# Kernel optimization log

Measured on AMD Instinct MI355X. Metric: run time of the kernel, lower is better.

The kernel has to match this reference:

```python
import jax, jax.numpy as jnp
import numpy as np

D_MODEL = 1024
NUM_HEADS = 16
NUM_KV_HEADS = 4
HEAD_DIM = D_MODEL // NUM_HEADS  # 64
THETA = 10000.0
MAX_SEQ_LEN = 4096


def _rope_tables(max_seq_len, d_k, theta):
    k_vec = jnp.arange(0, d_k, 2, dtype=jnp.float32) / d_k
    freq = 1.0 / (theta ** k_vec)                       # (d_k/2,)
    ang = jnp.arange(max_seq_len, dtype=jnp.float32)[:, None] * freq[None, :]
    return jnp.cos(ang), jnp.sin(ang)                   # each (max_seq_len, d_k/2)


def _apply_rope(x, pos, cos_table, sin_table):
    # x: (b, h, l, d), pos: (b, l)
    cos = cos_table[pos][:, None, :, :]                 # (b, 1, l, d/2)
    sin = sin_table[pos][:, None, :, :]
    even, odd = x[..., 0::2], x[..., 1::2]
    r1 = even * cos - odd * sin
    r2 = even * sin + odd * cos
    return jnp.stack([r1, r2], axis=-1).reshape(x.shape)  # interleave back


def setup_inputs() -> dict:
    key = jax.random.key(0)
    ks = jax.random.split(key, 6)
    B, L, D = 1, 4096, D_MODEL
    std = (2.0 / (D + D)) ** 0.5
    std_kv = (2.0 / (D + HEAD_DIM * NUM_KV_HEADS)) ** 0.5
    x = jax.random.normal(ks[0], (B, L, D), dtype=jnp.float32)
    Wq = jax.random.normal(ks[1], (D, D), dtype=jnp.float32) * std
    Wk = jax.random.normal(ks[2], (HEAD_DIM * NUM_KV_HEADS, D), dtype=jnp.float32) * std_kv
    Wv = jax.random.normal(ks[3], (HEAD_DIM * NUM_KV_HEADS, D), dtype=jnp.float32) * std_kv
    Wo = jax.random.normal(ks[4], (D, D), dtype=jnp.float32) * std
    token_positions = jnp.broadcast_to(jnp.arange(L, dtype=jnp.int32), (B, L))
    return {"x": x, "Wq": Wq, "Wk": Wk, "Wv": Wv, "Wo": Wo,
            "token_positions": token_positions}


def reference(x, Wq, Wk, Wv, Wo, token_positions):
    B, L, D = x.shape
    H, Hkv, Dh = NUM_HEADS, NUM_KV_HEADS, HEAD_DIM
    n_rep = H // Hkv
    cos_t, sin_t = _rope_tables(MAX_SEQ_LEN, Dh, THETA)

    q = (x @ Wq.T).reshape(B, L, H, Dh).transpose(0, 2, 1, 3)      # b h l d
    k = (x @ Wk.T).reshape(B, L, Hkv, Dh).transpose(0, 2, 1, 3)    # b g l d
    v = (x @ Wv.T).reshape(B, L, Hkv, Dh).transpose(0, 2, 1, 3)

    q = _apply_rope(q, token_positions, cos_t, sin_t)
    k = _apply_rope(k, token_positions, cos_t, sin_t)

    # GQA: group query heads by kv head
    qg = q.reshape(B, Hkv, n_rep, L, Dh)
    scores = jnp.einsum('bgrqd,bgkd->bgrqk', qg, k) / jnp.sqrt(jnp.float32(Dh))
    causal = jnp.tril(jnp.ones((L, L), dtype=bool))
    scores = jnp.where(causal, scores, -jnp.inf)
    weights = jax.nn.softmax(scores, axis=-1)
    out = jnp.einsum('bgrqk,bgkd->bgrqd', weights, v)              # b g r q d
    out = out.reshape(B, H, L, Dh).transpose(0, 2, 1, 3).reshape(B, L, D)
    return out @ Wo.T
```

## Files before the change

### kernel.cpp

```cpp
#include <hip/hip_runtime.h>
#include <hip/hip_bf16.h>
#include <math.h>

typedef __bf16 bf16;
typedef __bf16 v8bf __attribute__((ext_vector_type(8)));
typedef __bf16 v4bf __attribute__((ext_vector_type(4)));
typedef __bf16 v2bf __attribute__((ext_vector_type(2)));
typedef float f32x4 __attribute__((ext_vector_type(4)));
typedef float f32x16 __attribute__((ext_vector_type(16)));

#define L_SEQ 4096
#define DMODEL 1024
#define NHEADS 16
#define DH 64
#define NEG_BIG (-1e30f)
#define LN1E4_64 0.14391156f
#define SCL2 0.18033688f
#define DEFER_THR 8.0f

static __device__ __forceinline__ unsigned pkbf(float x, float y) {
    v2bf t; t[0] = (bf16)x; t[1] = (bf16)y;
    return __builtin_bit_cast(unsigned, t);
}

__global__ void convert_all(const float* __restrict__ x, const float* __restrict__ wq,
                            const float* __restrict__ wk, const float* __restrict__ wv,
                            const float* __restrict__ wo,
                            bf16* __restrict__ xb, bf16* __restrict__ wqkvb,
                            bf16* __restrict__ wob) {
    int i = (blockIdx.x * 256 + threadIdx.x) * 4;
    const float* src;
    bf16* dst;
    if (i < 4194304)      { src = x  + i;             dst = xb    + i; }
    else if (i < 5242880) { src = wq + (i - 4194304); dst = wqkvb + (i - 4194304); }
    else if (i < 5505024) { src = wk + (i - 5242880); dst = wqkvb + 1048576 + (i - 5242880); }
    else if (i < 5767168) { src = wv + (i - 5505024); dst = wqkvb + 1310720 + (i - 5505024); }
    else                  { src = wo + (i - 5767168); dst = wob   + (i - 5767168); }
    f32x4 v = *(const f32x4*)src;
    v4bf r;
#pragma unroll
    for (int j = 0; j < 4; j++) r[j] = (bf16)v[j];
    *(v4bf*)dst = r;
}

__global__ __launch_bounds__(512) void gemm_qkv(const bf16* __restrict__ A,
                                                const bf16* __restrict__ W,
                                                bf16* __restrict__ Qb,
                                                bf16* __restrict__ Kb,
                                                bf16* __restrict__ Vtg,
                                                const int* __restrict__ tp) {
    __shared__ bf16 As[128][68];
    __shared__ bf16 Bs[128][68];
    const int K = 1024;
    const int tid = threadIdx.x;
    const int w = tid >> 6, lane = tid & 63;
    const int quad = lane >> 4, l16 = lane & 15;
    const int wm = (w & 1) * 64, wn = (w >> 1) * 32;
    const int bm = blockIdx.y * 128, bn = blockIdx.x * 128;

    f32x4 acc[4][2];
#pragma unroll
    for (int mf = 0; mf < 4; mf++)
#pragma unroll
        for (int nf = 0; nf < 2; nf++) acc[mf][nf] = (f32x4){0.f, 0.f, 0.f, 0.f};

    const int sr = tid >> 2;
    const int scb = (tid & 3) * 16;

    v8bf pa0, pa1, pb0, pb1;
    {
        const bf16* ap = &A[(size_t)(bm + sr) * K + scb];
        const bf16* bp = &W[(size_t)(bn + sr) * K + scb];
        pa0 = *(const v8bf*)ap; pa1 = *(const v8bf*)(ap + 8);
        pb0 = *(const v8bf*)bp; pb1 = *(const v8bf*)(bp + 8);
        *(v8bf*)&As[sr][scb] = pa0; *(v8bf*)&As[sr][scb + 8] = pa1;
        *(v8bf*)&Bs[sr][scb] = pb0; *(v8bf*)&Bs[sr][scb + 8] = pb1;
    }

    for (int kt = 0; kt < K; kt += 64) {
        __syncthreads();
        const bool more = (kt + 64) < K;
        if (more) {
            const bf16* ap = &A[(size_t)(bm + sr) * K + kt + 64 + scb];
            const bf16* bp = &W[(size_t)(bn + sr) * K + kt + 64 + scb];
            pa0 = *(const v8bf*)ap; pa1 = *(const v8bf*)(ap + 8);
            pb0 = *(const v8bf*)bp; pb1 = *(const v8bf*)(bp + 8);
        }
#pragma unroll
        for (int kf = 0; kf < 2; kf++) {
            v8bf a[4], b[2];
#pragma unroll
            for (int mf = 0; mf < 4; mf++) a[mf] = *(v8bf*)&As[wm + mf * 16 + l16][kf * 32 + quad * 8];
#pragma unroll
            for (int nf = 0; nf < 2; nf++) b[nf] = *(v8bf*)&Bs[wn + nf * 16 + l16][kf * 32 + quad * 8];
#pragma unroll
            for (int mf = 0; mf < 4; mf++)
#pragma unroll
                for (int nf = 0; nf < 2; nf++)
                    acc[mf][nf] = __builtin_amdgcn_mfma_f32_16x16x32_bf16(a[mf], b[nf], acc[mf][nf], 0, 0, 0);
        }
        __syncthreads();
        if (more) {
            *(v8bf*)&As[sr][scb] = pa0; *(v8bf*)&As[sr][scb + 8] = pa1;
            *(v8bf*)&Bs[sr][scb] = pb0; *(v8bf*)&Bs[sr][scb + 8] = pb1;
        }
    }

    if (bn < 1024) {
#pragma unroll
        for (int mf = 0; mf < 4; mf++) {
            int pos_[4];
#pragma unroll
            for (int r = 0; r < 4; r++) pos_[r] = tp[bm + wm + mf * 16 + quad * 4 + r];
#pragma unroll
            for (int nf = 0; nf < 2; nf++) {
                const int col = bn + wn + nf * 16 + l16;
                float fr = __expf(-(float)((col & 63) & ~1) * LN1E4_64);
#pragma unroll
                for (int r = 0; r < 4; r++) {
                    float v = acc[mf][nf][r];
                    float sn, cs;
                    __sincosf((float)pos_[r] * fr, &sn, &cs);
                    float p = __shfl_xor(v, 1);
                    float res = (l16 & 1) ? (p * sn + v * cs) : (v * cs - p * sn);
                    int row = bm + wm + mf * 16 + quad * 4 + r;
                    Qb[(size_t)row * DMODEL + col] = (bf16)(res * SCL2);
                }
            }
        }
    } else if (bn < 1280) {
#pragma unroll
        for (int mf = 0; mf < 4; mf++) {
            int pos_[4];
#pragma unroll
            for (int r = 0; r < 4; r++) pos_[r] = tp[bm + wm + mf * 16 + quad * 4 + r];
#pragma unroll
            for (int nf = 0; nf < 2; nf++) {
                const int kcol = bn - 1024 + wn + nf * 16 + l16;
                float fr = __expf(-(float)((kcol & 63) & ~1) * LN1E4_64);
#pragma unroll
                for (int r = 0; r < 4; r++) {
                    float v = acc[mf][nf][r];
                    float sn, cs;
                    __sincosf((float)pos_[r] * fr, &sn, &cs);
                    float p = __shfl_xor(v, 1);
                    float res = (l16 & 1) ? (p * sn + v * cs) : (v * cs - p * sn);
                    int row = bm + wm + mf * 16 + quad * 4 + r;
                    Kb[(size_t)row * 256 + kcol] = (bf16)res;
                }
            }
        }
    } else {
#pragma unroll
        for (int mf = 0; mf < 4; mf++)
#pragma unroll
            for (int nf = 0; nf < 2; nf++) {
                v4bf pk;
#pragma unroll
                for (int r = 0; r < 4; r++) pk[r] = (bf16)acc[mf][nf][r];
                int vcol = bn - 1280 + wn + nf * 16 + l16;
                int row = bm + wm + mf * 16 + quad * 4;
                *(v4bf*)&Vtg[(size_t)vcol * L_SEQ + row] = pk;
            }
    }
}

__global__ __launch_bounds__(512) void gemm_out(const bf16* __restrict__ A,
                                                const bf16* __restrict__ W,
                                                float* __restrict__ C) {
    __shared__ bf16 As[128][68];
    __shared__ bf16 Bs[128][68];
    const int K = 1024, N = 1024;
    const int tid = threadIdx.x;
    const int w = tid >> 6, lane = tid & 63;
    const int quad = lane >> 4, l16 = lane & 15;
    const int wm = (w & 1) * 64, wn = (w >> 1) * 32;
    const int bm = blockIdx.y * 128, bn = blockIdx.x * 128;

    f32x4 acc[4][2];
#pragma unroll
    for (int mf = 0; mf < 4; mf++)
#pragma unroll
        for (int nf = 0; nf < 2; nf++) acc[mf][nf] = (f32x4){0.f, 0.f, 0.f, 0.f};

    const int sr = tid >> 2;
    const int scb = (tid & 3) * 16;

    v8bf pa0, pa1, pb0, pb1;
    {
        const bf16* ap = &A[(size_t)(bm + sr) * K + scb];
        const bf16* bp = &W[(size_t)(bn + sr) * K + scb];
        pa0 = *(const v8bf*)ap; pa1 = *(const v8bf*)(ap + 8);
        pb0 = *(const v8bf*)bp; pb1 = *(const v8bf*)(bp + 8);
        *(v8bf*)&As[sr][scb] = pa0; *(v8bf*)&As[sr][scb + 8] = pa1;
        *(v8bf*)&Bs[sr][scb] = pb0; *(v8bf*)&Bs[sr][scb + 8] = pb1;
    }

    for (int kt = 0; kt < K; kt += 64) {
        __syncthreads();
        const bool more = (kt + 64) < K;
        if (more) {
            const bf16* ap = &A[(size_t)(bm + sr) * K + kt + 64 + scb];
            const bf16* bp = &W[(size_t)(bn + sr) * K + kt + 64 + scb];
            pa0 = *(const v8bf*)ap; pa1 = *(const v8bf*)(ap + 8);
            pb0 = *(const v8bf*)bp; pb1 = *(const v8bf*)(bp + 8);
        }
#pragma unroll
        for (int kf = 0; kf < 2; kf++) {
            v8bf a[4], b[2];
#pragma unroll
            for (int mf = 0; mf < 4; mf++) a[mf] = *(v8bf*)&As[wm + mf * 16 + l16][kf * 32 + quad * 8];
#pragma unroll
            for (int nf = 0; nf < 2; nf++) b[nf] = *(v8bf*)&Bs[wn + nf * 16 + l16][kf * 32 + quad * 8];
#pragma unroll
            for (int mf = 0; mf < 4; mf++)
#pragma unroll
                for (int nf = 0; nf < 2; nf++)
                    acc[mf][nf] = __builtin_amdgcn_mfma_f32_16x16x32_bf16(a[mf], b[nf], acc[mf][nf], 0, 0, 0);
        }
        __syncthreads();
        if (more) {
            *(v8bf*)&As[sr][scb] = pa0; *(v8bf*)&As[sr][scb + 8] = pa1;
            *(v8bf*)&Bs[sr][scb] = pb0; *(v8bf*)&Bs[sr][scb + 8] = pb1;
        }
    }
#pragma unroll
    for (int mf = 0; mf < 4; mf++)
#pragma unroll
        for (int nf = 0; nf < 2; nf++)
#pragma unroll
            for (int r = 0; r < 4; r++) {
                int row = bm + wm + mf * 16 + quad * 4 + r;
                int col = bn + wn + nf * 16 + l16;
                C[(size_t)row * N + col] = acc[mf][nf][r];
            }
}

__global__ __launch_bounds__(256, 2) void flash10(const bf16* __restrict__ Q,
                                                  const bf16* __restrict__ Kb,
                                                  const bf16* __restrict__ Vtg,
                                                  bf16* __restrict__ O0,
                                                  bf16* __restrict__ O1,
                                                  float* __restrict__ ML) {
    __shared__ bf16 Ks[128][68];
    __shared__ bf16 Vt[64][132];
    const int h = blockIdx.y, kvh = h >> 2;
    const int bx = blockIdx.x;
    const int tid = threadIdx.x;
    const int w = tid >> 6, lane = tid & 63;
    const int l32 = lane & 31, hi = lane >> 5;
    const int krow = tid >> 1, kcb = (tid & 1) * 32;
    const int vr = tid >> 2, vcb = (tid & 3) * 32;

    for (int p = 0; p < 2; p++) {
        const int qb = p ? (31 - bx) : bx;
        const int T = qb + 1;
        const int k0 = p ? ((T + 1) >> 1) : 0;
        const int k1 = p ? T : ((T + 1) >> 1);
        bf16* Op = p ? O1 : O0;
        float* mlp = ML + (size_t)(p * NHEADS + h) * L_SEQ * 2;

        if (k0 >= k1) {
            for (int i = tid; i < 128 * 64; i += 256) {
                int rr = i >> 6, cc = i & 63;
                Op[(size_t)(qb * 128 + rr) * DMODEL + h * DH + cc] = (bf16)0.f;
            }
            if (tid < 128) {
                mlp[(qb * 128 + tid) * 2 + 0] = NEG_BIG;
                mlp[(qb * 128 + tid) * 2 + 1] = 0.f;
            }
            continue;
        }

        const int qrow = qb * 128 + w * 32 + l32;
        v8bf qf[4];
#pragma unroll
        for (int d16 = 0; d16 < 4; d16++)
            qf[d16] = *(const v8bf*)&Q[(size_t)qrow * DMODEL + h * DH + d16 * 16 + hi * 8];

        f32x16 oaccT[2];
#pragma unroll
        for (int d = 0; d < 2; d++)
#pragma unroll
            for (int r = 0; r < 16; r++) oaccT[d][r] = 0.f;
        float m_i = NEG_BIG, l_i = 0.f;

        v8bf kreg[4], vreg[4];
        {
            const bf16* ks = &Kb[(size_t)(k0 * 128 + krow) * 256 + kvh * DH + kcb];
            const bf16* vs = &Vtg[(size_t)(kvh * DH + vr) * L_SEQ + k0 * 128 + vcb];
#pragma unroll
            for (int u = 0; u < 4; u++) { kreg[u] = *(const v8bf*)&ks[8 * u]; vreg[u] = *(const v8bf*)&vs[8 * u]; }
            __syncthreads();
#pragma unroll
            for (int u = 0; u < 4; u++) { *(v8bf*)&Ks[krow][kcb + 8 * u] = kreg[u]; *(v8bf*)&Vt[vr][vcb + 8 * u] = vreg[u]; }
        }

        for (int kb = k0; kb < k1; kb++) {
            __syncthreads();
            if (kb + 1 < k1) {
                const bf16* ks = &Kb[(size_t)((kb + 1) * 128 + krow) * 256 + kvh * DH + kcb];
                const bf16* vs = &Vtg[(size_t)(kvh * DH + vr) * L_SEQ + (kb + 1) * 128 + vcb];
#pragma unroll
                for (int u = 0; u < 4; u++) { kreg[u] = *(const v8bf*)&ks[8 * u]; vreg[u] = *(const v8bf*)&vs[8 * u]; }
            }

            f32x16 s[4];
            __builtin_amdgcn_s_setprio(1);
#pragma unroll
            for (int n = 0; n < 4; n++) {
#pragma unroll
                for (int r = 0; r < 16; r++) s[n][r] = 0.f;
#pragma unroll
                for (int d16 = 0; d16 < 4; d16++) {
                    v8bf av = *(v8bf*)&Ks[n * 32 + l32][d16 * 16 + hi * 8];
                    s[n] = __builtin_amdgcn_mfma_f32_32x32x16_bf16(av, qf[d16], s[n], 0, 0, 0);
                }
            }
            __builtin_amdgcn_s_setprio(0);

            if (kb == qb) {
#pragma unroll
                for (int n = 0; n < 4; n++) {
                    int kbase = kb * 128 + n * 32 + 4 * hi;
#pragma unroll
                    for (int r = 0; r < 16; r++) {
                        int key = kbase + (r & 3) + 8 * (r >> 2);
                        if (key > qrow) s[n][r] = NEG_BIG;
                    }
                }
            }

            float mx = NEG_BIG;
#pragma unroll
            for (int n = 0; n < 4; n++)
#pragma unroll
                for (int r = 0; r < 16; r += 2)
                    mx = fmaxf(fmaxf(mx, s[n][r]), s[n][r + 1]);
            mx = fmaxf(mx, __shfl_xor(mx, 32));

            if (!__all(mx <= m_i + DEFER_THR)) {
                float mnew = fmaxf(m_i, mx);
                float alpha = exp2f(m_i - mnew);
                l_i *= alpha;
#pragma unroll
                for (int d = 0; d < 2; d++)
#pragma unroll
                    for (int r = 0; r < 16; r++) oaccT[d][r] *= alpha;
                m_i = mnew;
            }

            float rs = 0.f;
#pragma unroll
            for (int n = 0; n < 4; n++)
#pragma unroll
                for (int r = 0; r < 16; r++) {
                    float pv = exp2f(s[n][r] - m_i);
                    s[n][r] = pv;
                    rs += pv;
                }
            rs += __shfl_xor(rs, 32);
            l_i += rs;

            __builtin_amdgcn_s_setprio(1);
#pragma unroll
            for (int n = 0; n < 4; n++) {
#pragma unroll
                for (int u = 0; u < 2; u++) {
                    const int ro = u * 8;
                    unsigned a0 = pkbf(s[n][ro + 0], s[n][ro + 1]);
                    unsigned a1 = pkbf(s[n][ro + 2], s[n][ro + 3]);
                    unsigned b0 = pkbf(s[n][ro + 4], s[n][ro + 5]);
                    unsigned b1 = pkbf(s[n][ro + 6], s[n][ro + 7]);
#if __has_builtin(__builtin_amdgcn_permlane32_swap)
                    auto s0 = __builtin_amdgcn_permlane32_swap(a0, b0, false, false);
                    auto s1 = __builtin_amdgcn_permlane32_swap(a1, b1, false, false);
                    unsigned w0 = s0[0], w2 = s0[1], w1 = s1[0], w3 = s1[1];
#else
                    unsigned t0 = hi ? a0 : b0;
                    unsigned r0 = __shfl_xor(t0, 32);
                    unsigned w0 = hi ? r0 : a0, w2 = hi ? b0 : r0;
                    unsigned t1 = hi ? a1 : b1;
                    unsigned r1 = __shfl_xor(t1, 32);
                    unsigned w1 = hi ? r1 : a1, w3 = hi ? b1 : r1;
#endif
                    union { unsigned uu[4]; v8bf v; } pf;
                    pf.uu[0] = w0; pf.uu[1] = w1; pf.uu[2] = w2; pf.uu[3] = w3;
                    const int t = n * 2 + u;
#pragma unroll
                    for (int dblk = 0; dblk < 2; dblk++) {
                        v8bf av = *(v8bf*)&Vt[dblk * 32 + l32][t * 16 + hi * 8];
                        oaccT[dblk] = __builtin_amdgcn_mfma_f32_32x32x16_bf16(av, pf.v, oaccT[dblk], 0, 0, 0);
                    }
                }
            }
            __builtin_amdgcn_s_setprio(0);

            __syncthreads();
            if (kb + 1 < k1) {
#pragma unroll
                for (int u = 0; u < 4; u++) { *(v8bf*)&Ks[krow][kcb + 8 * u] = kreg[u]; *(v8bf*)&Vt[vr][vcb + 8 * u] = vreg[u]; }
            }
        }

#pragma unroll
        for (int dblk = 0; dblk < 2; dblk++)
#pragma unroll
            for (int r = 0; r < 16; r++) {
                int d = dblk * 32 + (r & 3) + 8 * (r >> 2) + 4 * hi;
                Ks[w * 32 + l32][d] = (bf16)oaccT[dblk][r];
            }
        asm volatile("s_waitcnt lgkmcnt(0)" ::: "memory");
        __builtin_amdgcn_sched_barrier(0);
#pragma unroll
        for (int i = 0; i < 4; i++) {
            int cc = (lane & 1) * 32 + i * 8;
            int rr = w * 32 + (lane >> 1);
            v8bf ov = *(v8bf*)&Ks[rr][cc];
            *(v8bf*)&Op[(size_t)(qb * 128 + rr) * DMODEL + h * DH + cc] = ov;
        }
        if (hi == 0) {
            mlp[qrow * 2 + 0] = m_i;
            mlp[qrow * 2 + 1] = l_i;
        }
    }
}

__global__ void combine(const bf16* __restrict__ O0, const bf16* __restrict__ O1,
                        const float* __restrict__ ML, bf16* __restrict__ Attn) {
    int gid = blockIdx.x * 256 + threadIdx.x;
    int row = gid >> 8;
    int cg = (gid & 255) * 4;
    int h = cg >> 6;
    const float* ml0 = ML + ((size_t)h * L_SEQ + row) * 2;
    const float* ml1 = ML + ((size_t)(NHEADS + h) * L_SEQ + row) * 2;
    float m0 = ml0[0], l0 = ml0[1], m1 = ml1[0], l1 = ml1[1];
    float m = fmaxf(m0, m1);
    float a0 = exp2f(m0 - m), a1 = exp2f(m1 - m);
    float inv = 1.f / (a0 * l0 + a1 * l1);
    v4bf o0 = *(const v4bf*)&O0[(size_t)row * DMODEL + cg];
    v4bf o1 = *(const v4bf*)&O1[(size_t)row * DMODEL + cg];
    v4bf res;
#pragma unroll
    for (int j = 0; j < 4; j++)
        res[j] = (bf16)((a0 * (float)o0[j] + a1 * (float)o1[j]) * inv);
    *(v4bf*)&Attn[(size_t)row * DMODEL + cg] = res;
}

extern "C" void kernel_launch(void* const* d_in, const int* in_sizes, int n_in,
                              void* d_out, int out_size, void* d_ws, size_t ws_size,
                              hipStream_t stream) {
    const float* x  = (const float*)d_in[0];
    const float* Wq = (const float*)d_in[1];
    const float* Wk = (const float*)d_in[2];
    const float* Wv = (const float*)d_in[3];
    const float* Wo = (const float*)d_in[4];
    const int*   tp = (const int*)d_in[5];
    float* out = (float*)d_out;

    bf16*  xb    = (bf16*)d_ws;
    bf16*  wqkvb = xb    + 4194304;
    bf16*  wob   = wqkvb + 1572864;
    bf16*  Qb    = wob   + 1048576;
    bf16*  Kb    = Qb    + 4194304;
    bf16*  Vtg   = Kb    + 1048576;
    float* MLf   = (float*)(Vtg + 1048576);
    bf16*  Attn  = xb;
    bf16*  O0    = (bf16*)d_out;
    bf16*  O1    = O0 + 4194304;

    convert_all<<<6656, 256, 0, stream>>>(x, Wq, Wk, Wv, Wo, xb, wqkvb, wob);
    gemm_qkv<<<dim3(12, 32), 512, 0, stream>>>(xb, wqkvb, Qb, Kb, Vtg, tp);
    flash10<<<dim3(32, NHEADS), 256, 0, stream>>>(Qb, Kb, Vtg, O0, O1, MLf);
    combine<<<4096, 256, 0, stream>>>(O0, O1, MLf, Attn);
    gemm_out<<<dim3(8, 32), 512, 0, stream>>>(Attn, wob, out);
}
```

Before: 200.1 us.

## Double-buffer GEMM LDS tiles, swap grid order, compute softmax row-sum via MFMA

Both GEMMs now use double-buffered shared-memory tiles, so the next tile is written into the alternate buffer and each k-step needs one barrier instead of two. The launch grids of the GEMMs and the attention kernel are transposed, so consecutive blocks walk along M or across heads, which changes L2 reuse of the weight and KV tiles. The attention kernel drops the scalar row-sum and cross-lane shuffle and instead accumulates the softmax denominator with an extra MFMA against a vector of ones. This adds MFMA work, accumulator registers and doubled LDS usage, which may reduce occupancy.

```diff
diff --git a/kernel.cpp b/kernel.cpp
--- a/kernel.cpp
+++ b/kernel.cpp
@@ -49,14 +49,14 @@
                                                 bf16* __restrict__ Kb,
                                                 bf16* __restrict__ Vtg,
                                                 const int* __restrict__ tp) {
-    __shared__ bf16 As[128][68];
-    __shared__ bf16 Bs[128][68];
+    __shared__ bf16 As[2][128][68];
+    __shared__ bf16 Bs[2][128][68];
     const int K = 1024;
     const int tid = threadIdx.x;
     const int w = tid >> 6, lane = tid & 63;
     const int quad = lane >> 4, l16 = lane & 15;
     const int wm = (w & 1) * 64, wn = (w >> 1) * 32;
-    const int bm = blockIdx.y * 128, bn = blockIdx.x * 128;
+    const int bm = blockIdx.x * 128, bn = blockIdx.y * 128;
 
     f32x4 acc[4][2];
 #pragma unroll
@@ -73,12 +73,13 @@
         const bf16* bp = &W[(size_t)(bn + sr) * K + scb];
         pa0 = *(const v8bf*)ap; pa1 = *(const v8bf*)(ap + 8);
         pb0 = *(const v8bf*)bp; pb1 = *(const v8bf*)(bp + 8);
-        *(v8bf*)&As[sr][scb] = pa0; *(v8bf*)&As[sr][scb + 8] = pa1;
-        *(v8bf*)&Bs[sr][scb] = pb0; *(v8bf*)&Bs[sr][scb + 8] = pb1;
-    }
-
+        *(v8bf*)&As[0][sr][scb] = pa0; *(v8bf*)&As[0][sr][scb + 8] = pa1;
+        *(v8bf*)&Bs[0][sr][scb] = pb0; *(v8bf*)&Bs[0][sr][scb + 8] = pb1;
+        __syncthreads();
+    }
+
+    int cur = 0;
     for (int kt = 0; kt < K; kt += 64) {
-        __syncthreads();
         const bool more = (kt + 64) < K;
         if (more) {
             const bf16* ap = &A[(size_t)(bm + sr) * K + kt + 64 + scb];
@@ -90,20 +91,21 @@
         for (int kf = 0; kf < 2; kf++) {
             v8bf a[4], b[2];
 #pragma unroll
-            for (int mf = 0; mf < 4; mf++) a[mf] = *(v8bf*)&As[wm + mf * 16 + l16][kf * 32 + quad * 8];
-#pragma unroll
-            for (int nf = 0; nf < 2; nf++) b[nf] = *(v8bf*)&Bs[wn + nf * 16 + l16][kf * 32 + quad * 8];
+            for (int mf = 0; mf < 4; mf++) a[mf] = *(v8bf*)&As[cur][wm + mf * 16 + l16][kf * 32 + quad * 8];
+#pragma unroll
+            for (int nf = 0; nf < 2; nf++) b[nf] = *(v8bf*)&Bs[cur][wn + nf * 16 + l16][kf * 32 + quad * 8];
 #pragma unroll
             for (int mf = 0; mf < 4; mf++)
 #pragma unroll
                 for (int nf = 0; nf < 2; nf++)
                     acc[mf][nf] = __builtin_amdgcn_mfma_f32_16x16x32_bf16(a[mf], b[nf], acc[mf][nf], 0, 0, 0);
         }
+        if (more) {
+            *(v8bf*)&As[cur ^ 1][sr][scb] = pa0; *(v8bf*)&As[cur ^ 1][sr][scb + 8] = pa1;
+            *(v8bf*)&Bs[cur ^ 1][sr][scb] = pb0; *(v8bf*)&Bs[cur ^ 1][sr][scb + 8] = pb1;
+        }
         __syncthreads();
-        if (more) {
-            *(v8bf*)&As[sr][scb] = pa0; *(v8bf*)&As[sr][scb + 8] = pa1;
-            *(v8bf*)&Bs[sr][scb] = pb0; *(v8bf*)&Bs[sr][scb + 8] = pb1;
-        }
+        cur ^= 1;
     }
 
     if (bn < 1024) {
@@ -168,14 +170,14 @@
 __global__ __launch_bounds__(512) void gemm_out(const bf16* __restrict__ A,
                                                 const bf16* __restrict__ W,
                                                 float* __restrict__ C) {
-    __shared__ bf16 As[128][68];
-    __shared__ bf16 Bs[128][68];
+    __shared__ bf16 As[2][128][68];
+    __shared__ bf16 Bs[2][128][68];
     const int K = 1024, N = 1024;
     const int tid = threadIdx.x;
     const int w = tid >> 6, lane = tid & 63;
     const int quad = lane >> 4, l16 = lane & 15;
     const int wm = (w & 1) * 64, wn = (w >> 1) * 32;
-    const int bm = blockIdx.y * 128, bn = blockIdx.x * 128;
+    const int bm = blockIdx.x * 128, bn = blockIdx.y * 128;
 
     f32x4 acc[4][2];
 #pragma unroll
@@ -192,12 +194,13 @@
         const bf16* bp = &W[(size_t)(bn + sr) * K + scb];
         pa0 = *(const v8bf*)ap; pa1 = *(const v8bf*)(ap + 8);
         pb0 = *(const v8bf*)bp; pb1 = *(const v8bf*)(bp + 8);
-        *(v8bf*)&As[sr][scb] = pa0; *(v8bf*)&As[sr][scb + 8] = pa1;
-        *(v8bf*)&Bs[sr][scb] = pb0; *(v8bf*)&Bs[sr][scb + 8] = pb1;
-    }
-
+        *(v8bf*)&As[0][sr][scb] = pa0; *(v8bf*)&As[0][sr][scb + 8] = pa1;
+        *(v8bf*)&Bs[0][sr][scb] = pb0; *(v8bf*)&Bs[0][sr][scb + 8] = pb1;
+        __syncthreads();
+    }
+
+    int cur = 0;
     for (int kt = 0; kt < K; kt += 64) {
-        __syncthreads();
         const bool more = (kt + 64) < K;
         if (more) {
             const bf16* ap = &A[(size_t)(bm + sr) * K + kt + 64 + scb];
@@ -209,20 +212,21 @@
         for (int kf = 0; kf < 2; kf++) {
             v8bf a[4], b[2];
 #pragma unroll
-            for (int mf = 0; mf < 4; mf++) a[mf] = *(v8bf*)&As[wm + mf * 16 + l16][kf * 32 + quad * 8];
-#pragma unroll
-            for (int nf = 0; nf < 2; nf++) b[nf] = *(v8bf*)&Bs[wn + nf * 16 + l16][kf * 32 + quad * 8];
+            for (int mf = 0; mf < 4; mf++) a[mf] = *(v8bf*)&As[cur][wm + mf * 16 + l16][kf * 32 + quad * 8];
+#pragma unroll
+            for (int nf = 0; nf < 2; nf++) b[nf] = *(v8bf*)&Bs[cur][wn + nf * 16 + l16][kf * 32 + quad * 8];
 #pragma unroll
             for (int mf = 0; mf < 4; mf++)
 #pragma unroll
                 for (int nf = 0; nf < 2; nf++)
                     acc[mf][nf] = __builtin_amdgcn_mfma_f32_16x16x32_bf16(a[mf], b[nf], acc[mf][nf], 0, 0, 0);
         }
+        if (more) {
+            *(v8bf*)&As[cur ^ 1][sr][scb] = pa0; *(v8bf*)&As[cur ^ 1][sr][scb + 8] = pa1;
+            *(v8bf*)&Bs[cur ^ 1][sr][scb] = pb0; *(v8bf*)&Bs[cur ^ 1][sr][scb + 8] = pb1;
+        }
         __syncthreads();
-        if (more) {
-            *(v8bf*)&As[sr][scb] = pa0; *(v8bf*)&As[sr][scb + 8] = pa1;
-            *(v8bf*)&Bs[sr][scb] = pb0; *(v8bf*)&Bs[sr][scb + 8] = pb1;
-        }
+        cur ^= 1;
     }
 #pragma unroll
     for (int mf = 0; mf < 4; mf++)
@@ -236,7 +240,7 @@
             }
 }
 
-__global__ __launch_bounds__(256, 2) void flash10(const bf16* __restrict__ Q,
+__global__ __launch_bounds__(256, 2) void flash11(const bf16* __restrict__ Q,
                                                   const bf16* __restrict__ Kb,
                                                   const bf16* __restrict__ Vtg,
                                                   bf16* __restrict__ O0,
@@ -244,13 +248,17 @@
                                                   float* __restrict__ ML) {
     __shared__ bf16 Ks[128][68];
     __shared__ bf16 Vt[64][132];
-    const int h = blockIdx.y, kvh = h >> 2;
-    const int bx = blockIdx.x;
+    const int h = blockIdx.x, kvh = h >> 2;
+    const int bx = blockIdx.y;
     const int tid = threadIdx.x;
     const int w = tid >> 6, lane = tid & 63;
     const int l32 = lane & 31, hi = lane >> 5;
     const int krow = tid >> 1, kcb = (tid & 1) * 32;
     const int vr = tid >> 2, vcb = (tid & 3) * 32;
+
+    v8bf ones;
+#pragma unroll
+    for (int j = 0; j < 8; j++) ones[j] = (bf16)1.0f;
 
     for (int p = 0; p < 2; p++) {
         const int qb = p ? (31 - bx) : bx;
@@ -278,12 +286,14 @@
         for (int d16 = 0; d16 < 4; d16++)
             qf[d16] = *(const v8bf*)&Q[(size_t)qrow * DMODEL + h * DH + d16 * 16 + hi * 8];
 
-        f32x16 oaccT[2];
+        f32x16 oaccT[2], lacc;
 #pragma unroll
         for (int d = 0; d < 2; d++)
 #pragma unroll
             for (int r = 0; r < 16; r++) oaccT[d][r] = 0.f;
-        float m_i = NEG_BIG, l_i = 0.f;
+#pragma unroll
+        for (int r = 0; r < 16; r++) lacc[r] = 0.f;
+        float m_i = NEG_BIG;
 
         v8bf kreg[4], vreg[4];
         {
@@ -342,7 +352,8 @@
             if (!__all(mx <= m_i + DEFER_THR)) {
                 float mnew = fmaxf(m_i, mx);
                 float alpha = exp2f(m_i - mnew);
-                l_i *= alpha;
+#pragma unroll
+                for (int r = 0; r < 16; r++) lacc[r] *= alpha;
 #pragma unroll
                 for (int d = 0; d < 2; d++)
 #pragma unroll
@@ -350,17 +361,11 @@
                 m_i = mnew;
             }
 
-            float rs = 0.f;
 #pragma unroll
             for (int n = 0; n < 4; n++)
 #pragma unroll
-                for (int r = 0; r < 16; r++) {
-                    float pv = exp2f(s[n][r] - m_i);
-                    s[n][r] = pv;
-                    rs += pv;
-                }
-            rs += __shfl_xor(rs, 32);
-            l_i += rs;
+                for (int r = 0; r < 16; r++)
+                    s[n][r] = exp2f(s[n][r] - m_i);
 
             __builtin_amdgcn_s_setprio(1);
 #pragma unroll
@@ -392,6 +397,7 @@
                         v8bf av = *(v8bf*)&Vt[dblk * 32 + l32][t * 16 + hi * 8];
                         oaccT[dblk] = __builtin_amdgcn_mfma_f32_32x32x16_bf16(av, pf.v, oaccT[dblk], 0, 0, 0);
                     }
+                    lacc = __builtin_amdgcn_mfma_f32_32x32x16_bf16(ones, pf.v, lacc, 0, 0, 0);
                 }
             }
             __builtin_amdgcn_s_setprio(0);
@@ -421,7 +427,7 @@
         }
         if (hi == 0) {
             mlp[qrow * 2 + 0] = m_i;
-            mlp[qrow * 2 + 1] = l_i;
+            mlp[qrow * 2 + 1] = lacc[0];
         }
     }
 }
@@ -470,8 +476,8 @@
     bf16*  O1    = O0 + 4194304;
 
     convert_all<<<6656, 256, 0, stream>>>(x, Wq, Wk, Wv, Wo, xb, wqkvb, wob);
-    gemm_qkv<<<dim3(12, 32), 512, 0, stream>>>(xb, wqkvb, Qb, Kb, Vtg, tp);
-    flash10<<<dim3(32, NHEADS), 256, 0, stream>>>(Qb, Kb, Vtg, O0, O1, MLf);
+    gemm_qkv<<<dim3(32, 12), 512, 0, stream>>>(xb, wqkvb, Qb, Kb, Vtg, tp);
+    flash11<<<dim3(NHEADS, 32), 256, 0, stream>>>(Qb, Kb, Vtg, O0, O1, MLf);
     combine<<<4096, 256, 0, stream>>>(O0, O1, MLf, Attn);
-    gemm_out<<<dim3(8, 32), 512, 0, stream>>>(Attn, wob, out);
-}
+    gemm_out<<<dim3(32, 8), 512, 0, stream>>>(Attn, wob, out);
+}
```

Result: no change. 198.4 us (-0.8%).
